# Kernel optimization log

Hardware: AMD Instinct MI355X
Metric: run time of the kernel (lower is better)

Reference implementation:

```python
import jax, jax.numpy as jnp
import numpy as np

N_NODES = 50000
N_EDGES = 800000
D = 128
BN_EPS = 1e-5


def _bn(x, gamma, beta):
    # BatchNorm1d in training mode: biased batch stats over node axis
    m = jnp.mean(x, axis=0)
    v = jnp.mean((x - m) ** 2, axis=0)
    return gamma * (x - m) * jax.lax.rsqrt(v + BN_EPS) + beta


def setup_inputs() -> dict:
    key = jax.random.key(0)
    ks = jax.random.split(key, 8)
    feats = jax.random.normal(ks[0], (N_NODES, D), dtype=jnp.float32)
    src = jax.random.randint(ks[1], (N_EDGES,), 0, N_NODES, dtype=jnp.int32)
    dst = jax.random.randint(ks[2], (N_EDGES,), 0, N_NODES, dtype=jnp.int32)
    s = 1.0 / np.sqrt(D)
    W1 = jax.random.uniform(ks[3], (D, D), jnp.float32, -s, s)
    b1 = jax.random.uniform(ks[4], (D,), jnp.float32, -s, s)
    W2 = jax.random.uniform(ks[5], (D, D), jnp.float32, -s, s)
    b2 = jax.random.uniform(ks[6], (D,), jnp.float32, -s, s)
    ones = jnp.ones((D,), jnp.float32)
    zeros = jnp.zeros((D,), jnp.float32)
    return {
        "feats": feats, "src": src, "dst": dst,
        "W1": W1, "b1": b1, "g1": ones, "be1": zeros,
        "W2": W2, "b2": b2, "g2": ones, "be2": zeros,
        "g3": ones, "be3": zeros,
    }


def reference(feats, src, dst, W1, b1, g1, be1, W2, b2, g2, be2, g3, be3):
    # GIN 'max' aggregation: for each dst node, elementwise max over source feats
    msgs = feats[src]  # [E, D] gather (memory-bound)
    agg = jax.ops.segment_max(msgs, dst, num_segments=N_NODES)
    # DGL gives 0 for nodes with no in-edges; segment_max gives -inf
    agg = jnp.where(jnp.isfinite(agg), agg, 0.0)
    h = feats + agg  # (1 + eps) * feats + agg, eps = 0
    # GINNodeFunc: Linear -> BN -> ReLU -> Linear -> BN -> ReLU
    h = jax.nn.relu(_bn(h @ W1 + b1, g1, be1))
    h = jax.nn.relu(_bn(h @ W2 + b2, g2, be2))
    # outer BN; dropout treated as identity (eval / deterministic baseline)
    return _bn(h, g3, be3)
```

## Files before the change

### kernel.cpp

```cpp
#include <hip/hip_runtime.h>
#include <stdint.h>


#define NN 50000
#define NE 800000
#define DD 128
#define BN_EPS 1e-5f
#define NB 1563
#define CAPB 768
#define NBK 64
#define EPB 12500

typedef short bf16x8 __attribute__((ext_vector_type(8)));
typedef float f32x4 __attribute__((ext_vector_type(4)));

__device__ __forceinline__ float bf2f(unsigned short u) {
    return __uint_as_float(((unsigned int)u) << 16);
}
__device__ __forceinline__ unsigned short f2bf(float f) {
    unsigned int u = __float_as_uint(f);
    u += 0x7fffu + ((u >> 16) & 1u);
    return (unsigned short)(u >> 16);
}
__device__ __forceinline__ float plo(unsigned int p) { return bf2f((unsigned short)(p & 0xffffu)); }
__device__ __forceinline__ float phi(unsigned int p) { return bf2f((unsigned short)(p >> 16)); }

__global__ __launch_bounds__(256) void k_prep(
    const float* __restrict__ feats, unsigned int* __restrict__ fb,
    const float* __restrict__ W1, const float* __restrict__ W2,
    unsigned short* __restrict__ Wt1, unsigned short* __restrict__ Wt2,
    unsigned int* __restrict__ bcur)
{
    int g = blockIdx.x * 256 + threadIdx.x;
    float4 v = *reinterpret_cast<const float4*>(feats + (size_t)g * 4);
    uint2 o;
    o.x = (unsigned int)f2bf(v.x) | ((unsigned int)f2bf(v.y) << 16);
    o.y = (unsigned int)f2bf(v.z) | ((unsigned int)f2bf(v.w) << 16);
    *reinterpret_cast<uint2*>(fb + (size_t)g * 2) = o;
    if (g < 16384) {
        int row = g >> 7, col = g & 127;
        Wt1[col * DD + row] = f2bf(W1[g]);
    } else if (g < 32768) {
        int h = g - 16384;
        int row = h >> 7, col = h & 127;
        Wt2[col * DD + row] = f2bf(W2[h]);
    }
    if (g < NB) bcur[(size_t)g * 16] = (unsigned int)g * CAPB;
}

__global__ __launch_bounds__(1024) void k_bin(
    const int* __restrict__ src, const int* __restrict__ dst,
    unsigned int* __restrict__ bcur, unsigned int* __restrict__ tmp)
{
    __shared__ unsigned int words[EPB];
    __shared__ unsigned short loff[EPB];
    __shared__ unsigned int lhist[NB];
    __shared__ unsigned int lbase[NB];
    int tid = threadIdx.x;
    int e0 = blockIdx.x * EPB;
    for (int c = tid; c < NB; c += 1024) lhist[c] = 0u;
    __syncthreads();
    for (int i = tid; i < EPB; i += 1024) {
        int d = dst[e0 + i];
        int s = src[e0 + i];
        words[i] = ((unsigned int)s << 16) | (unsigned int)d;
        loff[i] = (unsigned short)atomicAdd(&lhist[d >> 5], 1u);
    }
    __syncthreads();
    for (int c = tid; c < NB; c += 1024) {
        unsigned int cnt = lhist[c];
        lbase[c] = cnt ? atomicAdd(&bcur[(size_t)c * 16], cnt) : 0u;
    }
    __syncthreads();
    for (int i = tid; i < EPB; i += 1024) {
        unsigned int w = words[i];
        int b = (int)((w & 0xffffu) >> 5);
        unsigned int pos = lbase[b] + (unsigned int)loff[i];
        if (pos < (unsigned int)(b + 1) * CAPB) tmp[pos] = w;
    }
}

__global__ __launch_bounds__(512) void k_aggmax(
    const unsigned int* __restrict__ F,
    const unsigned int* __restrict__ tmp,
    const unsigned int* __restrict__ bcur,
    unsigned int* __restrict__ h0)
{
    __shared__ unsigned int sorted[CAPB];
    __shared__ unsigned int hist[32];
    __shared__ unsigned int hbase[33];
    int tid = threadIdx.x;
    int b = blockIdx.x;
    if (tid < 32) hist[tid] = 0u;
    __syncthreads();
    unsigned int rb = (unsigned int)b * CAPB;
    unsigned int cnt = bcur[(size_t)b * 16] - rb;
    if (cnt > CAPB) cnt = CAPB;

    unsigned int wreg[2]; unsigned short lo[2]; int nw = 0;
    for (unsigned int i = tid; i < cnt; i += 512) {
        unsigned int ww = tmp[rb + i];
        wreg[nw] = ww;
        lo[nw] = (unsigned short)atomicAdd(&hist[ww & 31], 1u);
        nw++;
    }
    __syncthreads();
    if (tid == 0) {
        unsigned int acc = 0;
#pragma unroll
        for (int i = 0; i < 32; ++i) { hbase[i] = acc; acc += hist[i]; }
        hbase[32] = acc;
    }
    __syncthreads();
    for (int k = 0; k < nw; ++k)
        sorted[hbase[wreg[k] & 31] + (unsigned int)lo[k]] = wreg[k];
    __syncthreads();

    int wave = tid >> 6, lane = tid & 63;
    int n0 = b * 32;
#pragma unroll 1
    for (int dd = wave * 4; dd < wave * 4 + 4; ++dd) {
        int n = n0 + dd;
        if (n >= NN) continue;
        int st = (int)hbase[dd], en = (int)hbase[dd + 1];
        float m0 = -3.0e38f, m1 = -3.0e38f;
        int i = st;
        for (; i + 4 <= en; i += 4) {
            unsigned int w0 = sorted[i], w1 = sorted[i + 1];
            unsigned int w2 = sorted[i + 2], w3 = sorted[i + 3];
            unsigned int u0 = F[(w0 >> 16) * 64 + lane];
            unsigned int u1 = F[(w1 >> 16) * 64 + lane];
            unsigned int u2 = F[(w2 >> 16) * 64 + lane];
            unsigned int u3 = F[(w3 >> 16) * 64 + lane];
            m0 = fmaxf(m0, fmaxf(fmaxf(plo(u0), plo(u1)), fmaxf(plo(u2), plo(u3))));
            m1 = fmaxf(m1, fmaxf(fmaxf(phi(u0), phi(u1)), fmaxf(phi(u2), phi(u3))));
        }
        for (; i < en; ++i) {
            unsigned int ww = sorted[i];
            unsigned int u = F[(ww >> 16) * 64 + lane];
            m0 = fmaxf(m0, plo(u));
            m1 = fmaxf(m1, phi(u));
        }
        if (en == st) { m0 = 0.f; m1 = 0.f; }
        unsigned int pf = F[n * 64 + lane];
        h0[n * 64 + lane] = (unsigned int)f2bf(plo(pf) + m0) |
                            ((unsigned int)f2bf(phi(pf) + m1) << 16);
    }
}

template <int FUSE>
__global__ __launch_bounds__(512) void k_gemm(
    const unsigned short* __restrict__ X, const unsigned short* __restrict__ Wt,
    const float* __restrict__ bias, const float* __restrict__ pa,
    const float* __restrict__ pc, unsigned short* __restrict__ Y,
    float* __restrict__ partials)
{
    __shared__ float lsum[128], lsq[128];
    int tid = threadIdx.x;
    if (tid < 128) { lsum[tid] = 0.f; lsq[tid] = 0.f; }
    __syncthreads();
    int wave = tid >> 6, lane = tid & 63;
    int quad = lane >> 4, l16 = lane & 15;
    int m0 = blockIdx.x * 64 + (wave >> 1) * 16;
    int nh = (wave & 1) * 64;
    int myrow = m0 + l16;
    int kq = quad * 8;

    f32x4 acc[4];
#pragma unroll
    for (int j = 0; j < 4; ++j)
#pragma unroll
        for (int r = 0; r < 4; ++r) acc[j][r] = 0.f;

#pragma unroll
    for (int k0 = 0; k0 < 128; k0 += 32) {
        bf16x8 a;
        if (myrow < NN) {
            a = *reinterpret_cast<const bf16x8*>(X + myrow * DD + k0 + kq);
            if (FUSE) {
                float4 av0 = *reinterpret_cast<const float4*>(pa + k0 + kq);
                float4 av1 = *reinterpret_cast<const float4*>(pa + k0 + kq + 4);
                float4 cv0 = *reinterpret_cast<const float4*>(pc + k0 + kq);
                float4 cv1 = *reinterpret_cast<const float4*>(pc + k0 + kq + 4);
                float fa[8] = {av0.x, av0.y, av0.z, av0.w, av1.x, av1.y, av1.z, av1.w};
                float fc[8] = {cv0.x, cv0.y, cv0.z, cv0.w, cv1.x, cv1.y, cv1.z, cv1.w};
#pragma unroll
                for (int j = 0; j < 8; ++j) {
                    float v = fmaxf(fa[j] * bf2f((unsigned short)a[j]) + fc[j], 0.f);
                    a[j] = (short)f2bf(v);
                }
            }
        } else {
#pragma unroll
            for (int j = 0; j < 8; ++j) a[j] = 0;
        }
#pragma unroll
        for (int j = 0; j < 4; ++j) {
            bf16x8 bb = *reinterpret_cast<const bf16x8*>(Wt + (nh + j * 16 + l16) * DD + k0 + kq);
            acc[j] = __builtin_amdgcn_mfma_f32_16x16x32_bf16(a, bb, acc[j], 0, 0, 0);
        }
    }

    int rbase = m0 + quad * 4;
#pragma unroll
    for (int j = 0; j < 4; ++j) {
        int col = nh + j * 16 + l16;
        float bcol = bias[col];
        float s = 0.f, q = 0.f;
#pragma unroll
        for (int r = 0; r < 4; ++r) {
            int row = rbase + r;
            if (row < NN) {
                float v = acc[j][r] + bcol;
                Y[row * DD + col] = f2bf(v);
                s += v;
                q += v * v;
            }
        }
        s += __shfl_xor(s, 16, 64);
        s += __shfl_xor(s, 32, 64);
        q += __shfl_xor(q, 16, 64);
        q += __shfl_xor(q, 32, 64);
        if (quad == 0) {
            atomicAdd(&lsum[col], s);
            atomicAdd(&lsq[col], q);
        }
    }
    __syncthreads();
    if (tid < 128) {
        partials[blockIdx.x * 256 + tid] = lsum[tid];
        partials[blockIdx.x * 256 + 128 + tid] = lsq[tid];
    }
}

__global__ void k_redparams(const float* __restrict__ partials, int nblk,
                            const float* __restrict__ g, const float* __restrict__ be,
                            float* __restrict__ a, float* __restrict__ c) {
    __shared__ float ls[256], lq[256];
    int t = threadIdx.x;
    int col = blockIdx.x;
    float s = 0.f, q = 0.f;
    for (int i = t; i < nblk; i += 256) {
        s += partials[i * 256 + col];
        q += partials[i * 256 + 128 + col];
    }
    ls[t] = s; lq[t] = q;
    __syncthreads();
    for (int off = 128; off > 0; off >>= 1) {
        if (t < off) { ls[t] += ls[t + off]; lq[t] += lq[t + off]; }
        __syncthreads();
    }
    if (t == 0) {
        float mean = ls[0] / (float)NN;
        float var = fmaxf(lq[0] / (float)NN - mean * mean, 0.f);
        float av = g[col] * rsqrtf(var + BN_EPS);
        a[col] = av;
        c[col] = be[col] - mean * av;
    }
}

__global__ __launch_bounds__(256) void k_zstats(
    const unsigned short* __restrict__ Y2, const float* __restrict__ a2,
    const float* __restrict__ c2, float* __restrict__ partials)
{
    __shared__ float ls[256], lq[256];
    int t = threadIdx.x;
    int col = t & 127, half = t >> 7;
    float av = a2[col], cv = c2[col];
    float s = 0.f, q = 0.f;
    for (int row = blockIdx.x * 2 + half; row < NN; row += gridDim.x * 2) {
        float z = fmaxf(av * bf2f(Y2[row * DD + col]) + cv, 0.f);
        s += z;
        q += z * z;
    }
    ls[t] = s;
    lq[t] = q;
    __syncthreads();
    if (t < 128) {
        partials[blockIdx.x * 256 + t] = ls[t] + ls[t + 128];
        partials[blockIdx.x * 256 + 128 + t] = lq[t] + lq[t + 128];
    }
}

__global__ __launch_bounds__(256) void k_out(
    const unsigned short* __restrict__ Y2, const float* __restrict__ a2,
    const float* __restrict__ c2, const float* __restrict__ a3,
    const float* __restrict__ c3, float* __restrict__ out)
{
    int g = blockIdx.x * 256 + threadIdx.x;
    int base = g * 4;
    int c0 = base & 127;
    uint2 p = *reinterpret_cast<const uint2*>(Y2 + base);
    float4 av2 = *reinterpret_cast<const float4*>(a2 + c0);
    float4 cv2 = *reinterpret_cast<const float4*>(c2 + c0);
    float4 av3 = *reinterpret_cast<const float4*>(a3 + c0);
    float4 cv3 = *reinterpret_cast<const float4*>(c3 + c0);
    float z0 = fmaxf(av2.x * plo(p.x) + cv2.x, 0.f);
    float z1 = fmaxf(av2.y * phi(p.x) + cv2.y, 0.f);
    float z2 = fmaxf(av2.z * plo(p.y) + cv2.z, 0.f);
    float z3 = fmaxf(av2.w * phi(p.y) + cv2.w, 0.f);
    float4 o;
    o.x = av3.x * z0 + cv3.x;
    o.y = av3.y * z1 + cv3.y;
    o.z = av3.z * z2 + cv3.z;
    o.w = av3.w * z3 + cv3.w;
    *reinterpret_cast<float4*>(out + base) = o;
}

extern "C" void kernel_launch(void* const* d_in, const int* in_sizes, int n_in,
                              void* d_out, int out_size, void* d_ws, size_t ws_size,
                              hipStream_t stream) {
    (void)in_sizes; (void)n_in; (void)out_size; (void)ws_size;
    const float* feats = (const float*)d_in[0];
    const int* src = (const int*)d_in[1];
    const int* dst = (const int*)d_in[2];
    const float* W1 = (const float*)d_in[3];
    const float* b1 = (const float*)d_in[4];
    const float* g1 = (const float*)d_in[5];
    const float* be1 = (const float*)d_in[6];
    const float* W2 = (const float*)d_in[7];
    const float* b2 = (const float*)d_in[8];
    const float* g2 = (const float*)d_in[9];
    const float* be2 = (const float*)d_in[10];
    const float* g3 = (const float*)d_in[11];
    const float* be3 = (const float*)d_in[12];
    float* out = (float*)d_out;

    char* p = (char*)d_ws;
    auto alloc = [&](size_t n) { char* r = p; p += (n + 255) & ~(size_t)255; return r; };
    unsigned int* fb = (unsigned int*)alloc((size_t)NN * 64 * 4);
    unsigned int* h0 = (unsigned int*)alloc((size_t)NN * 64 * 4);
    unsigned int* bcur = (unsigned int*)alloc((size_t)NB * 16 * 4);
    unsigned int* tmp = (unsigned int*)alloc((size_t)NB * CAPB * 4);
    unsigned short* Y1 = (unsigned short*)alloc((size_t)NN * DD * 2);
    unsigned short* Y2 = (unsigned short*)alloc((size_t)NN * DD * 2);
    unsigned short* Wt1 = (unsigned short*)alloc((size_t)DD * DD * 2);
    unsigned short* Wt2 = (unsigned short*)alloc((size_t)DD * DD * 2);
    float* partials = (float*)alloc((size_t)784 * 256 * 4);
    float* a1 = (float*)alloc(DD * 4); float* c1 = (float*)alloc(DD * 4);
    float* a2 = (float*)alloc(DD * 4); float* c2 = (float*)alloc(DD * 4);
    float* a3 = (float*)alloc(DD * 4); float* c3 = (float*)alloc(DD * 4);

    k_prep<<<6250, 256, 0, stream>>>(feats, fb, W1, W2, Wt1, Wt2, bcur);
    k_bin<<<NBK, 1024, 0, stream>>>(src, dst, bcur, tmp);
    k_aggmax<<<NB, 512, 0, stream>>>(fb, tmp, bcur, h0);
    k_gemm<0><<<782, 512, 0, stream>>>((const unsigned short*)h0, Wt1, b1,
                                       nullptr, nullptr, Y1, partials);
    k_redparams<<<128, 256, 0, stream>>>(partials, 782, g1, be1, a1, c1);
    k_gemm<1><<<782, 512, 0, stream>>>(Y1, Wt2, b2, a1, c1, Y2, partials);
    k_redparams<<<128, 256, 0, stream>>>(partials, 782, g2, be2, a2, c2);
    k_zstats<<<256, 256, 0, stream>>>(Y2, a2, c2, partials);
    k_redparams<<<128, 256, 0, stream>>>(partials, 256, g3, be3, a3, c3);
    k_out<<<6250, 256, 0, stream>>>(Y2, a2, c2, a3, c3, out);
}
```

Measured before the change: 258.5 us.

## Fuse max aggregation with first GEMM via shared-memory row tile

The max-aggregation kernel now keeps its 32 aggregated rows in padded shared memory and immediately runs the first MFMA GEMM, bias add and BN partial statistics on them. This removes the h0 intermediate write/read and one kernel launch. The cost is that each block does a smaller 32-row GEMM with reloads of the weights per block, plus twice as many partial-stat rows to reduce.

```diff
diff --git a/kernel.cpp b/kernel.cpp
--- a/kernel.cpp
+++ b/kernel.cpp
@@ -10,6 +10,7 @@
 #define CAPB 768
 #define NBK 64
 #define EPB 12500
+#define HS 68
 
 typedef short bf16x8 __attribute__((ext_vector_type(8)));
 typedef float f32x4 __attribute__((ext_vector_type(4)));
@@ -80,18 +81,22 @@
     }
 }
 
-__global__ __launch_bounds__(512) void k_aggmax(
+__global__ __launch_bounds__(512) void k_agg_gemm(
     const unsigned int* __restrict__ F,
     const unsigned int* __restrict__ tmp,
     const unsigned int* __restrict__ bcur,
-    unsigned int* __restrict__ h0)
+    const unsigned short* __restrict__ Wt, const float* __restrict__ bias,
+    unsigned short* __restrict__ Y, float* __restrict__ partials)
 {
     __shared__ unsigned int sorted[CAPB];
     __shared__ unsigned int hist[32];
     __shared__ unsigned int hbase[33];
+    __shared__ unsigned int hrow[32 * HS];
+    __shared__ float lsum[128], lsq[128];
     int tid = threadIdx.x;
     int b = blockIdx.x;
     if (tid < 32) hist[tid] = 0u;
+    if (tid >= 256 && tid < 384) { lsum[tid - 256] = 0.f; lsq[tid - 256] = 0.f; }
     __syncthreads();
     unsigned int rb = (unsigned int)b * CAPB;
     unsigned int cnt = bcur[(size_t)b * 16] - rb;
@@ -121,7 +126,7 @@
 #pragma unroll 1
     for (int dd = wave * 4; dd < wave * 4 + 4; ++dd) {
         int n = n0 + dd;
-        if (n >= NN) continue;
+        if (n >= NN) { hrow[dd * HS + lane] = 0u; continue; }
         int st = (int)hbase[dd], en = (int)hbase[dd + 1];
         float m0 = -3.0e38f, m1 = -3.0e38f;
         int i = st;
@@ -143,13 +148,63 @@
         }
         if (en == st) { m0 = 0.f; m1 = 0.f; }
         unsigned int pf = F[n * 64 + lane];
-        h0[n * 64 + lane] = (unsigned int)f2bf(plo(pf) + m0) |
-                            ((unsigned int)f2bf(phi(pf) + m1) << 16);
-    }
-}
-
-template <int FUSE>
-__global__ __launch_bounds__(512) void k_gemm(
+        hrow[dd * HS + lane] = (unsigned int)f2bf(plo(pf) + m0) |
+                               ((unsigned int)f2bf(phi(pf) + m1) << 16);
+    }
+    __syncthreads();
+
+    int quad = lane >> 4, l16 = lane & 15;
+    int rl = (wave >> 2) * 16 + l16;
+    int nh = (wave & 3) * 32;
+    int kq = quad * 8;
+    f32x4 acc[2];
+#pragma unroll
+    for (int j = 0; j < 2; ++j)
+#pragma unroll
+        for (int r = 0; r < 4; ++r) acc[j][r] = 0.f;
+#pragma unroll
+    for (int k0 = 0; k0 < 128; k0 += 32) {
+        bf16x8 a = *reinterpret_cast<const bf16x8*>(&hrow[rl * HS + ((k0 + kq) >> 1)]);
+#pragma unroll
+        for (int j = 0; j < 2; ++j) {
+            bf16x8 bb = *reinterpret_cast<const bf16x8*>(Wt + (nh + j * 16 + l16) * DD + k0 + kq);
+            acc[j] = __builtin_amdgcn_mfma_f32_16x16x32_bf16(a, bb, acc[j], 0, 0, 0);
+        }
+    }
+
+    int rbase = n0 + (wave >> 2) * 16 + quad * 4;
+#pragma unroll
+    for (int j = 0; j < 2; ++j) {
+        int col = nh + j * 16 + l16;
+        float bcol = bias[col];
+        float s = 0.f, q = 0.f;
+#pragma unroll
+        for (int r = 0; r < 4; ++r) {
+            int row = rbase + r;
+            if (row < NN) {
+                float v = acc[j][r] + bcol;
+                Y[row * DD + col] = f2bf(v);
+                s += v;
+                q += v * v;
+            }
+        }
+        s += __shfl_xor(s, 16, 64);
+        s += __shfl_xor(s, 32, 64);
+        q += __shfl_xor(q, 16, 64);
+        q += __shfl_xor(q, 32, 64);
+        if (quad == 0) {
+            atomicAdd(&lsum[col], s);
+            atomicAdd(&lsq[col], q);
+        }
+    }
+    __syncthreads();
+    if (tid < 128) {
+        partials[blockIdx.x * 256 + tid] = lsum[tid];
+        partials[blockIdx.x * 256 + 128 + tid] = lsq[tid];
+    }
+}
+
+__global__ __launch_bounds__(512) void k_gemm2(
     const unsigned short* __restrict__ X, const unsigned short* __restrict__ Wt,
     const float* __restrict__ bias, const float* __restrict__ pa,
     const float* __restrict__ pc, unsigned short* __restrict__ Y,
@@ -177,18 +232,16 @@
         bf16x8 a;
         if (myrow < NN) {
             a = *reinterpret_cast<const bf16x8*>(X + myrow * DD + k0 + kq);
-            if (FUSE) {
-                float4 av0 = *reinterpret_cast<const float4*>(pa + k0 + kq);
-                float4 av1 = *reinterpret_cast<const float4*>(pa + k0 + kq + 4);
-                float4 cv0 = *reinterpret_cast<const float4*>(pc + k0 + kq);
-                float4 cv1 = *reinterpret_cast<const float4*>(pc + k0 + kq + 4);
-                float fa[8] = {av0.x, av0.y, av0.z, av0.w, av1.x, av1.y, av1.z, av1.w};
-                float fc[8] = {cv0.x, cv0.y, cv0.z, cv0.w, cv1.x, cv1.y, cv1.z, cv1.w};
-#pragma unroll
-                for (int j = 0; j < 8; ++j) {
-                    float v = fmaxf(fa[j] * bf2f((unsigned short)a[j]) + fc[j], 0.f);
-                    a[j] = (short)f2bf(v);
-                }
+            float4 av0 = *reinterpret_cast<const float4*>(pa + k0 + kq);
+            float4 av1 = *reinterpret_cast<const float4*>(pa + k0 + kq + 4);
+            float4 cv0 = *reinterpret_cast<const float4*>(pc + k0 + kq);
+            float4 cv1 = *reinterpret_cast<const float4*>(pc + k0 + kq + 4);
+            float fa[8] = {av0.x, av0.y, av0.z, av0.w, av1.x, av1.y, av1.z, av1.w};
+            float fc[8] = {cv0.x, cv0.y, cv0.z, cv0.w, cv1.x, cv1.y, cv1.z, cv1.w};
+#pragma unroll
+            for (int j = 0; j < 8; ++j) {
+                float v = fmaxf(fa[j] * bf2f((unsigned short)a[j]) + fc[j], 0.f);
+                a[j] = (short)f2bf(v);
             }
         } else {
 #pragma unroll
@@ -329,25 +382,22 @@
     char* p = (char*)d_ws;
     auto alloc = [&](size_t n) { char* r = p; p += (n + 255) & ~(size_t)255; return r; };
     unsigned int* fb = (unsigned int*)alloc((size_t)NN * 64 * 4);
-    unsigned int* h0 = (unsigned int*)alloc((size_t)NN * 64 * 4);
     unsigned int* bcur = (unsigned int*)alloc((size_t)NB * 16 * 4);
     unsigned int* tmp = (unsigned int*)alloc((size_t)NB * CAPB * 4);
     unsigned short* Y1 = (unsigned short*)alloc((size_t)NN * DD * 2);
     unsigned short* Y2 = (unsigned short*)alloc((size_t)NN * DD * 2);
     unsigned short* Wt1 = (unsigned short*)alloc((size_t)DD * DD * 2);
     unsigned short* Wt2 = (unsigned short*)alloc((size_t)DD * DD * 2);
-    float* partials = (float*)alloc((size_t)784 * 256 * 4);
+    float* partials = (float*)alloc((size_t)1568 * 256 * 4);
     float* a1 = (float*)alloc(DD * 4); float* c1 = (float*)alloc(DD * 4);
     float* a2 = (float*)alloc(DD * 4); float* c2 = (float*)alloc(DD * 4);
     float* a3 = (float*)alloc(DD * 4); float* c3 = (float*)alloc(DD * 4);
 
     k_prep<<<6250, 256, 0, stream>>>(feats, fb, W1, W2, Wt1, Wt2, bcur);
     k_bin<<<NBK, 1024, 0, stream>>>(src, dst, bcur, tmp);
-    k_aggmax<<<NB, 512, 0, stream>>>(fb, tmp, bcur, h0);
-    k_gemm<0><<<782, 512, 0, stream>>>((const unsigned short*)h0, Wt1, b1,
-                                       nullptr, nullptr, Y1, partials);
-    k_redparams<<<128, 256, 0, stream>>>(partials, 782, g1, be1, a1, c1);
-    k_gemm<1><<<782, 512, 0, stream>>>(Y1, Wt2, b2, a1, c1, Y2, partials);
+    k_agg_gemm<<<NB, 512, 0, stream>>>(fb, tmp, bcur, Wt1, b1, Y1, partials);
+    k_redparams<<<128, 256, 0, stream>>>(partials, NB, g1, be1, a1, c1);
+    k_gemm2<<<782, 512, 0, stream>>>(Y1, Wt2, b2, a1, c1, Y2, partials);
     k_redparams<<<128, 256, 0, stream>>>(partials, 782, g2, be2, a2, c2);
     k_zstats<<<256, 256, 0, stream>>>(Y2, a2, c2, partials);
     k_redparams<<<128, 256, 0, stream>>>(partials, 256, g3, be3, a3, c3);
```

Result: faster. 252.3 us (-2.4%).
